# Kernel optimization log

Measured on AMD Instinct MI355X. Metric: run time of the kernel, lower is better.

## Reference

```python
import jax, jax.numpy as jnp
import numpy as np

# ---- module hyperparameters (from init_kwargs) ----
N_REPL = 4      # n
NUM_FM = 32
D = 2
PRD = 2
K_SZ = 2 * D + 1
ALPHA = 0.1
ETA = 0.1
THETA = 0.1
EPS = 1e-10


def symm_pad(x, p):
    # faithful to torch symm_pad: sequential in-place border reflection
    x = x.at[..., :p, :].set(jnp.flip(x[..., p:2 * p, :], axis=-2))
    x = x.at[..., -p:, :].set(jnp.flip(x[..., -2 * p:-p, :], axis=-2))
    x = x.at[..., :, :p].set(jnp.flip(x[..., :, p:2 * p], axis=-1))
    x = x.at[..., :, -p:].set(jnp.flip(x[..., :, -2 * p:-p], axis=-1))
    return x


def pad_activations(A, prd=PRD, d=D):
    H, W = A.shape[-2], A.shape[-1]
    pz = jnp.zeros(A.shape[:-2] + (prd * d + H, prd * d + W), A.dtype)
    pz = pz.at[..., prd:-prd, prd:-prd].set(A)
    return symm_pad(pz, 2 * prd)


def minmax_on_fm(x):
    # min-max normalize each feature map (last two dims) to [0,1]
    mn = x.min(axis=(-2, -1), keepdims=True)
    mx = x.max(axis=(-2, -1), keepdims=True)
    return (x - mn) / (mx - mn + EPS)


def softmax_on_fm(x):
    sh = x.shape
    return jax.nn.softmax(x.reshape(sh[:-2] + (-1,)), axis=-1).reshape(sh)


def softmax_minmax_scaled(x):
    return softmax_on_fm(minmax_on_fm(x))


def conv2d(x, w):
    # x: (B, Cin, H, W), w: (Cout, Cin, k, k), valid conv
    return jax.lax.conv_general_dilated(
        x, w, window_strides=(1, 1), padding='VALID',
        dimension_numbers=('NCHW', 'OIHW', 'NCHW'))


def setup_inputs() -> dict:
    key = jax.random.key(0)
    kA, kK, kN = jax.random.split(key, 3)
    C = N_REPL * NUM_FM
    A = jax.random.uniform(kA, (16, NUM_FM, 56, 56), jnp.float32)
    # K initialized as softmax_on_fm(rand), matching __init__
    K = softmax_on_fm(jax.random.uniform(kK, (C, C, K_SZ, K_SZ), jnp.float32))
    noise = jax.random.normal(kN, (16, C, 56, 56), jnp.float32)
    return {"A": A, "K": K, "noise": noise}


def reference(A, K, noise):
    B, num_fm, H, W = A.shape
    n, d, prd, k = N_REPL, D, PRD, K_SZ
    C = n * num_fm

    A = symm_pad(A, prd)                              # (B, num_fm, H, W)
    Ab = jnp.tile(A, (1, n, 1, 1))                    # (B, C, H, W)
    Ab = jnp.clip(Ab + ETA * noise, 0.0)
    pA = pad_activations(Ab)                          # (B, C, H+4, W+4)

    # torch does K.transpose_(0,1) in place; K1 is the post-transpose K
    K1 = jnp.swapaxes(K, 0, 1)
    L = conv2d(pA, minmax_on_fm(K1)) / num_fm         # (B, C, H, W)
    L = softmax_minmax_scaled(L)

    # winner-take-all across the n replicas of each feature map
    s = (Ab + L).sum(axis=(-2, -1)).reshape(B, n, num_fm)
    winners = jnp.argmax(jnp.swapaxes(s, 1, 2), axis=-1)          # (B, num_fm)
    fm_idx = num_fm * winners + jnp.arange(num_fm)                # (B, num_fm)
    win_mask = jnp.zeros((B, C), Ab.dtype).at[
        jnp.arange(B)[:, None], fm_idx].set(1.0)                  # 1 at winning channels

    # ---- Hebbian K update: per-offset masked cross-correlation ----
    Am = Ab * win_mask[:, :, None, None]  # zero losing *source* channels
    cols = []
    for x in range(k):
        xo = -d + x
        rows = []
        for y in range(k):
            yo = -d + y
            src = Am[:, :, max(0, xo):H + min(xo, 0), max(0, yo):W + min(yo, 0)]
            tgt = Ab[:, :, max(0, -xo):H + min(-xo, 0), max(0, -yo):W + min(-yo, 0)]
            rows.append(jnp.einsum('bchw,bahw->ca', src, tgt) / (C * B))
        cols.append(jnp.stack(rows, axis=-1))        # (C, C, k) over y
    K_change = jnp.stack(cols, axis=-2)              # (C, C, k, k) indexed [c,a,x,y]

    K2 = (1.0 - ALPHA) * K1 + ALPHA * minmax_on_fm(K_change)

    # ---- second lateral pass with losing channels zeroed ----
    A2 = Ab * win_mask[:, :, None, None]
    # torch zeroes only diagonal filters K[c,c] of losing c per sample; since the
    # corresponding input channels of A2 are exactly zero, a single shared-weight
    # conv is mathematically identical.
    L2 = conv2d(pad_activations(A2), minmax_on_fm(jnp.swapaxes(K2, 0, 1))) / num_fm

    gather = lambda X: jnp.take_along_axis(X, fm_idx[:, :, None, None], axis=1)
    O = gather(A2) + THETA * gather(L2)              # (B, num_fm, H, W)
    return O
```

## Files before the change

### kernel.cpp

```cpp
#include <hip/hip_runtime.h>


typedef __attribute__((ext_vector_type(8))) short short8;
typedef __attribute__((ext_vector_type(4))) float floatx4;

#define EPSF 1e-10f

__device__ __forceinline__ int map60(int r) {
  return r < 4 ? 5 - r : (r < 56 ? r - 2 : 109 - r);
}
__device__ __forceinline__ unsigned short f2bf(float x) {
  unsigned int u = __float_as_uint(x);
  u += 0x7fff + ((u >> 16) & 1);
  return (unsigned short)(u >> 16);
}
__device__ __forceinline__ float bf2f(unsigned int h) {
  return __uint_as_float((h & 0xffffu) << 16);
}
__device__ __forceinline__ short8 u4_to_s8(uint4 v) {
  union { uint4 u; short8 s; } cv;
  cv.u = v;
  return cv.s;
}

__global__ __launch_bounds__(256) void k1_build(const float* __restrict__ A,
                                                const float* __restrict__ noise,
                                                unsigned short* __restrict__ Abf,
                                                float* __restrict__ s) {
  int bc = blockIdx.x;
  int b = bc >> 7, c = bc & 127;
  int fm = c & 31;
  const float* Abase = A + (size_t)(b * 32 + fm) * 3136;
  const float* nz = noise + (size_t)bc * 3136;
  unsigned short* outb = Abf + 256 + (size_t)bc * 3840;
  float local = 0.f;
  for (int q = threadIdx.x; q < 960; q += 256) {
    int r = q >> 4, qc = q & 15, col0 = qc << 2;
    int h = r - 2;
    float v0, v1, v2, v3;
    if (r < 2 || r > 57 || qc == 15) {
      v0 = v1 = v2 = v3 = 0.f;
    } else if (r >= 4 && r <= 55 && qc >= 1 && qc <= 13) {
      int w0 = col0 - 2;
      const float* ap = Abase + h * 56 + w0;
      const float* np = nz + h * 56 + w0;
      float2 a0 = *reinterpret_cast<const float2*>(ap);
      float2 a1 = *reinterpret_cast<const float2*>(ap + 2);
      float2 n0 = *reinterpret_cast<const float2*>(np);
      float2 n1 = *reinterpret_cast<const float2*>(np + 2);
      v0 = fmaxf(a0.x + 0.1f * n0.x, 0.f);
      v1 = fmaxf(a0.y + 0.1f * n0.y, 0.f);
      v2 = fmaxf(a1.x + 0.1f * n1.x, 0.f);
      v3 = fmaxf(a1.y + 0.1f * n1.y, 0.f);
    } else {
      float vv[4];
      int hh = h < 2 ? 3 - h : (h >= 54 ? 107 - h : h);
#pragma unroll
      for (int j = 0; j < 4; j++) {
        int w = col0 + j - 2;
        float v = 0.f;
        if ((unsigned)w < 56u) {
          int ww = w < 2 ? 3 - w : (w >= 54 ? 107 - w : w);
          v = fmaxf(Abase[hh * 56 + ww] + 0.1f * nz[h * 56 + w], 0.f);
        }
        vv[j] = v;
      }
      v0 = vv[0]; v1 = vv[1]; v2 = vv[2]; v3 = vv[3];
    }
    local += v0 + v1 + v2 + v3;
    uint2 w;
    w.x = (unsigned)f2bf(v0) | ((unsigned)f2bf(v1) << 16);
    w.y = (unsigned)f2bf(v2) | ((unsigned)f2bf(v3) << 16);
    *reinterpret_cast<uint2*>(outb + r * 64 + col0) = w;
  }
  int lane = threadIdx.x & 63, wid = threadIdx.x >> 6;
  float v = local;
  for (int off = 32; off; off >>= 1) v += __shfl_down(v, off, 64);
  __shared__ float red[4];
  if (lane == 0) red[wid] = v;
  __syncthreads();
  if (threadIdx.x == 0) s[bc] = red[0] + red[1] + red[2] + red[3];
}

__global__ __launch_bounds__(512) void k2_winners(const float* __restrict__ s,
                                                  int* __restrict__ fm_idx,
                                                  int* __restrict__ cmask,
                                                  unsigned short* __restrict__ Abf) {
  int t = threadIdx.x;
  {
    int b = t >> 5, f = t & 31;
    float best = s[b * 128 + f];
    int bn = 0;
    for (int n = 1; n < 4; n++) {
      float v = s[b * 128 + n * 32 + f];
      if (v > best) { best = v; bn = n; }
    }
    fm_idx[t] = bn * 32 + f;
  }
  if (t < 256) Abf[t] = 0;
  if (t >= 256) Abf[256 + 7864320 + (t - 256)] = 0;
  __syncthreads();
  if (t < 128) {
    int m = 0;
    for (int b = 0; b < 16; b++)
      if (fm_idx[b * 32 + (t & 31)] == t) m |= (1 << b);
    cmask[t] = m;
  }
}

__global__ __launch_bounds__(256) void k2t_transpose(const unsigned short* __restrict__ Abf,
                                                     const int* __restrict__ fm_idx,
                                                     unsigned short* __restrict__ T) {
  __shared__ int win[32];
  int b = blockIdx.x / 15, chunk = blockIdx.x % 15;
  if (threadIdx.x < 32) win[threadIdx.x] = fm_idx[b * 32 + threadIdx.x];
  __syncthreads();
  int p = chunk * 256 + threadIdx.x;
  int r = p >> 6, s2 = p & 63;
  int mr = map60(r) + 2;
  int ms = (s2 < 60) ? map60(s2) + 2 : -1;
  unsigned int out[16];
#pragma unroll
  for (int gp = 0; gp < 16; gp++) {
    unsigned short v0 = 0, v1 = 0;
    if (ms >= 0) {
      v0 = Abf[256 + ((size_t)(b * 128) + win[2 * gp]) * 3840 + mr * 64 + ms];
      v1 = Abf[256 + ((size_t)(b * 128) + win[2 * gp + 1]) * 3840 + mr * 64 + ms];
    }
    out[gp] = (unsigned)v0 | ((unsigned)v1 << 16);
  }
  uint4* dst = reinterpret_cast<uint4*>(T + (size_t)b * 122880 + (size_t)p * 32);
#pragma unroll
  for (int q = 0; q < 4; q++) {
    uint4 u;
    u.x = out[4 * q]; u.y = out[4 * q + 1]; u.z = out[4 * q + 2]; u.w = out[4 * q + 3];
    dst[q] = u;
  }
}

__global__ __launch_bounds__(256) void k3_mfma(const unsigned short* __restrict__ Abf,
                                               const int* __restrict__ fm_idx,
                                               float* __restrict__ Kc_b) {
  int bx = blockIdx.x;
  int b = bx & 15;
  int rr = bx >> 4;
  int kh = rr & 1, mt = (rr >> 1) & 1, nt = rr >> 2;
  int wave = threadIdx.x >> 6, lane = threadIdx.x & 63;
  int al = lane & 15, quad = lane >> 4;
  int g0 = mt * 16, a0 = nt * 16;
  int k0 = kh * 1920 + wave * 480;
  floatx4 acc[5][5];
#pragma unroll
  for (int i = 0; i < 5; i++)
#pragma unroll
    for (int j = 0; j < 5; j++) acc[i][j] = (floatx4){0.f, 0.f, 0.f, 0.f};
  int c = fm_idx[b * 32 + g0 + al];
  const unsigned short* pA = Abf + 256 + (size_t)(b * 128 + c) * 3840 + k0 + quad * 8;
  const unsigned short* pB = Abf + 256 + (size_t)(b * 128 + a0 + al) * 3840 + k0 + quad * 8;
  for (int ks = 0; ks < 15; ks++) {
    short8 afr = *reinterpret_cast<const short8*>(pA);
#pragma unroll
    for (int dj = 0; dj < 5; dj++) {
      const unsigned short* bb = pB + 64 * (dj - 2);
      uint2 L = *reinterpret_cast<const uint2*>(bb - 4);
      uint4 M = *reinterpret_cast<const uint4*>(bb);
      uint2 R = *reinterpret_cast<const uint2*>(bb + 8);
      unsigned ab0 = __builtin_amdgcn_alignbit(M.x, L.y, 16);
      unsigned ab1 = __builtin_amdgcn_alignbit(M.y, M.x, 16);
      unsigned ab2 = __builtin_amdgcn_alignbit(M.z, M.y, 16);
      unsigned ab3 = __builtin_amdgcn_alignbit(M.w, M.z, 16);
      unsigned ab4 = __builtin_amdgcn_alignbit(R.x, M.w, 16);
      acc[0][dj] = __builtin_amdgcn_mfma_f32_16x16x32_bf16(
          afr, u4_to_s8((uint4){L.y, M.x, M.y, M.z}), acc[0][dj], 0, 0, 0);
      acc[1][dj] = __builtin_amdgcn_mfma_f32_16x16x32_bf16(
          afr, u4_to_s8((uint4){ab0, ab1, ab2, ab3}), acc[1][dj], 0, 0, 0);
      acc[2][dj] = __builtin_amdgcn_mfma_f32_16x16x32_bf16(
          afr, u4_to_s8((uint4){M.x, M.y, M.z, M.w}), acc[2][dj], 0, 0, 0);
      acc[3][dj] = __builtin_amdgcn_mfma_f32_16x16x32_bf16(
          afr, u4_to_s8((uint4){ab1, ab2, ab3, ab4}), acc[3][dj], 0, 0, 0);
      acc[4][dj] = __builtin_amdgcn_mfma_f32_16x16x32_bf16(
          afr, u4_to_s8((uint4){M.y, M.z, M.w, R.x}), acc[4][dj], 0, 0, 0);
    }
    pA += 32;
    pB += 32;
  }
  __shared__ float red[6400];
  float* myrow = red + lane * 100;
  if (wave == 0) {
#pragma unroll
    for (int di = 0; di < 5; di++)
#pragma unroll
      for (int dj = 0; dj < 5; dj++)
#pragma unroll
        for (int r = 0; r < 4; r++) myrow[(di * 5 + dj) * 4 + r] = acc[di][dj][r];
  }
  __syncthreads();
#pragma unroll
  for (int w = 1; w < 4; w++) {
    if (wave == w) {
#pragma unroll
      for (int di = 0; di < 5; di++)
#pragma unroll
        for (int dj = 0; dj < 5; dj++)
#pragma unroll
          for (int r = 0; r < 4; r++) myrow[(di * 5 + dj) * 4 + r] += acc[di][dj][r];
    }
    __syncthreads();
  }
  if (wave == 0) {
    int slot = b * 2 + kh;
#pragma unroll
    for (int di = 0; di < 5; di++)
#pragma unroll
      for (int dj = 0; dj < 5; dj++) {
        int t_out = 24 - (dj * 5 + di);
#pragma unroll
        for (int r = 0; r < 4; r++) {
          int g = g0 + quad * 4 + r;
          Kc_b[(((size_t)slot * 32 + g) * 128 + (a0 + al)) * 25 + t_out] =
              myrow[(di * 5 + dj) * 4 + r] * (1.0f / 2048.0f);
        }
      }
  }
}

__global__ __launch_bounds__(256) void k4_weights(const float* __restrict__ Kc_b,
                                                  const float* __restrict__ K,
                                                  const int* __restrict__ cmask,
                                                  unsigned short* __restrict__ W2g) {
  int gid = blockIdx.x * 256 + threadIdx.x;
  int o = gid >> 7, i = gid & 127;
  int mi = cmask[i], mo = cmask[o];
  float kc[25];
#pragma unroll
  for (int t = 0; t < 25; t++) kc[t] = 0.f;
  for (int slot = 0; slot < 32; slot++) {
    if ((mi >> (slot >> 1)) & 1) {
      const float* p = Kc_b + (((size_t)slot * 32 + (i & 31)) * 128 + o) * 25;
#pragma unroll
      for (int t = 0; t < 25; t++) kc[t] += p[t];
    }
  }
  float mn = 1e30f, mx = -1e30f;
#pragma unroll
  for (int t = 0; t < 25; t++) { mn = fminf(mn, kc[t]); mx = fmaxf(mx, kc[t]); }
  float d1 = mx - mn + EPSF;
  const float* kp = K + ((size_t)o * 128 + i) * 25;
  float k2[25], mn2 = 1e30f, mx2 = -1e30f;
#pragma unroll
  for (int t = 0; t < 25; t++) {
    k2[t] = 0.9f * kp[t] + 0.1f * ((kc[t] - mn) / d1);
    mn2 = fminf(mn2, k2[t]);
    mx2 = fmaxf(mx2, k2[t]);
  }
  float d2 = mx2 - mn2 + EPSF;
  unsigned short wb[25];
#pragma unroll
  for (int t = 0; t < 25; t++) wb[t] = f2bf((k2[t] - mn2) / d2);
  int mw = mo & mi;
  int f = o & 31, g = i & 31;
  while (mw) {
    int b = __ffs(mw) - 1;
    mw &= mw - 1;
    unsigned short* dst = W2g + ((size_t)(b * 25) * 32 + f) * 32 + g;
#pragma unroll
    for (int t = 0; t < 25; t++) dst[(size_t)t * 1024] = wb[t];
  }
}

__global__ __launch_bounds__(64) void k5_mfma(const unsigned short* __restrict__ W2g,
                                              const unsigned short* __restrict__ T,
                                              const unsigned short* __restrict__ Abf,
                                              const int* __restrict__ fm_idx,
                                              float* __restrict__ O) {
  int bx = blockIdx.x;
  int rg = bx % 14;
  int mtb = bx / 14;
  int mt = mtb & 1, b = mtb >> 1;
  int lane = threadIdx.x, al = lane & 15, quad = lane >> 4;
  int fm = mt * 16 + al;
  short8 afr[25];
#pragma unroll
  for (int t = 0; t < 25; t++)
    afr[t] = *reinterpret_cast<const short8*>(
        W2g + ((size_t)((b * 25 + t) * 32 + fm) << 5) + quad * 8);
  int orow[4];
#pragma unroll
  for (int r = 0; r < 4; r++) orow[r] = fm_idx[b * 32 + mt * 16 + quad * 4 + r];
  const unsigned short* Tb = T + (size_t)b * 122880;
  for (int rr = 0; rr < 4; rr++) {
    int row = 2 + rg * 4 + rr;
    for (int pair = 0; pair < 2; pair++) {
      int px0 = row * 64 + pair * 32 + al;
      floatx4 acca = (floatx4){0.f, 0.f, 0.f, 0.f};
      floatx4 accb = (floatx4){0.f, 0.f, 0.f, 0.f};
#pragma unroll
      for (int t = 0; t < 25; t++) {
        int off = (t / 5 - 2) * 64 + (t % 5) - 2;
        const short8* pb = reinterpret_cast<const short8*>(
            Tb + (ptrdiff_t)(px0 + off) * 32 + quad * 8);
        short8 b0 = pb[0];
        short8 b1 = pb[64];
        acca = __builtin_amdgcn_mfma_f32_16x16x32_bf16(afr[t], b0, acca, 0, 0, 0);
        accb = __builtin_amdgcn_mfma_f32_16x16x32_bf16(afr[t], b1, accb, 0, 0, 0);
      }
      int h = row - 2;
#pragma unroll
      for (int half = 0; half < 2; half++) {
        floatx4 acc = half ? accb : acca;
        int cc = pair * 32 + half * 16 + al;
        if (cc >= 2 && cc < 58) {
          int w = cc - 2;
          int px = row * 64 + cc;
#pragma unroll
          for (int r = 0; r < 4; r++) {
            int f = mt * 16 + quad * 4 + r;
            float base = bf2f(Abf[256 + (size_t)(b * 128 + orow[r]) * 3840 + px]);
            O[(size_t)(b * 32 + f) * 3136 + h * 56 + w] = base + acc[r] * (0.1f / 32.0f);
          }
        }
      }
    }
  }
}

extern "C" void kernel_launch(void* const* d_in, const int* in_sizes, int n_in,
                              void* d_out, int out_size, void* d_ws, size_t ws_size,
                              hipStream_t stream) {
  const float* A = (const float*)d_in[0];
  const float* K = (const float*)d_in[1];
  const float* noise = (const float*)d_in[2];
  float* O = (float*)d_out;

  float* ws = (float*)d_ws;
  unsigned short* Abf = (unsigned short*)ws;
  float* s = ws + 3932416;
  int* fm_idx = (int*)(ws + 3934464);
  int* cmask = (int*)(ws + 3934976);
  float* Kc_b = ws + 3935104;
  unsigned short* T = (unsigned short*)(ws + 7211904);
  unsigned short* W2g = (unsigned short*)(ws + 8194944);

  k1_build<<<2048, 256, 0, stream>>>(A, noise, Abf, s);
  k2_winners<<<1, 512, 0, stream>>>(s, fm_idx, cmask, Abf);
  k2t_transpose<<<240, 256, 0, stream>>>(Abf, fm_idx, T);
  k3_mfma<<<512, 256, 0, stream>>>(Abf, fm_idx, Kc_b);
  k4_weights<<<64, 256, 0, stream>>>(Kc_b, K, cmask, W2g);
  k5_mfma<<<448, 64, 0, stream>>>(W2g, T, Abf, fm_idx, O);
}
```

Baseline: 186.5 us.

## Reuse B-window registers across k-steps in correlation MFMA kernel

Exploits the fact that the 5 row-shifted B windows overlap across consecutive k-steps (stride 32 vs row stride 64): keeps even/odd register windows, shifts them down every two steps and loads only one new row pair, instead of reloading all five windows every step. Also prefetches the next A fragment, fully unrolls the k-loop and sets launch_bounds min 2 blocks. Cuts global/L1 load traffic in exchange for much higher register pressure (60 window regs plus 100 accumulators), which may cause spills or lower occupancy.

New measurement: 196.7 us. 5.5% more time.

```diff
diff --git a/kernel.cpp b/kernel.cpp
--- a/kernel.cpp
+++ b/kernel.cpp
@@ -138,13 +138,13 @@
   }
 }
 
-__global__ __launch_bounds__(256) void k3_mfma(const unsigned short* __restrict__ Abf,
-                                               const int* __restrict__ fm_idx,
-                                               float* __restrict__ Kc_b) {
+__global__ __launch_bounds__(256, 2) void k3_mfma(const unsigned short* __restrict__ Abf,
+                                                  const int* __restrict__ fm_idx,
+                                                  float* __restrict__ Kc_b) {
   int bx = blockIdx.x;
   int b = bx & 15;
-  int rr = bx >> 4;
-  int kh = rr & 1, mt = (rr >> 1) & 1, nt = rr >> 2;
+  int rblk = bx >> 4;
+  int kh = rblk & 1, mt = (rblk >> 1) & 1, nt = rblk >> 2;
   int wave = threadIdx.x >> 6, lane = threadIdx.x & 63;
   int al = lane & 15, quad = lane >> 4;
   int g0 = mt * 16, a0 = nt * 16;
@@ -155,35 +155,65 @@
 #pragma unroll
     for (int j = 0; j < 5; j++) acc[i][j] = (floatx4){0.f, 0.f, 0.f, 0.f};
   int c = fm_idx[b * 32 + g0 + al];
-  const unsigned short* pA = Abf + 256 + (size_t)(b * 128 + c) * 3840 + k0 + quad * 8;
-  const unsigned short* pB = Abf + 256 + (size_t)(b * 128 + a0 + al) * 3840 + k0 + quad * 8;
-  for (int ks = 0; ks < 15; ks++) {
-    short8 afr = *reinterpret_cast<const short8*>(pA);
+  const unsigned short* pA0 = Abf + 256 + (size_t)(b * 128 + c) * 3840 + k0 + quad * 8;
+  const unsigned short* pB0 = Abf + 256 + (size_t)(b * 128 + a0 + al) * 3840 + k0 + quad * 8;
+
+  auto loadwin = [&](unsigned* W, const unsigned short* ptr) {
+    W[0] = *reinterpret_cast<const unsigned*>(ptr - 2);
+    uint4 m = *reinterpret_cast<const uint4*>(ptr);
+    W[1] = m.x; W[2] = m.y; W[3] = m.z; W[4] = m.w;
+    W[5] = *reinterpret_cast<const unsigned*>(ptr + 8);
+  };
+  auto dostep = [&](unsigned (&W)[5][6], short8 afr) {
 #pragma unroll
     for (int dj = 0; dj < 5; dj++) {
-      const unsigned short* bb = pB + 64 * (dj - 2);
-      uint2 L = *reinterpret_cast<const uint2*>(bb - 4);
-      uint4 M = *reinterpret_cast<const uint4*>(bb);
-      uint2 R = *reinterpret_cast<const uint2*>(bb + 8);
-      unsigned ab0 = __builtin_amdgcn_alignbit(M.x, L.y, 16);
-      unsigned ab1 = __builtin_amdgcn_alignbit(M.y, M.x, 16);
-      unsigned ab2 = __builtin_amdgcn_alignbit(M.z, M.y, 16);
-      unsigned ab3 = __builtin_amdgcn_alignbit(M.w, M.z, 16);
-      unsigned ab4 = __builtin_amdgcn_alignbit(R.x, M.w, 16);
+      unsigned d0 = W[dj][0], d1 = W[dj][1], d2 = W[dj][2], d3 = W[dj][3],
+               d4 = W[dj][4], d5 = W[dj][5];
+      unsigned ab0 = __builtin_amdgcn_alignbit(d1, d0, 16);
+      unsigned ab1 = __builtin_amdgcn_alignbit(d2, d1, 16);
+      unsigned ab2 = __builtin_amdgcn_alignbit(d3, d2, 16);
+      unsigned ab3 = __builtin_amdgcn_alignbit(d4, d3, 16);
+      unsigned ab4 = __builtin_amdgcn_alignbit(d5, d4, 16);
       acc[0][dj] = __builtin_amdgcn_mfma_f32_16x16x32_bf16(
-          afr, u4_to_s8((uint4){L.y, M.x, M.y, M.z}), acc[0][dj], 0, 0, 0);
+          afr, u4_to_s8((uint4){d0, d1, d2, d3}), acc[0][dj], 0, 0, 0);
       acc[1][dj] = __builtin_amdgcn_mfma_f32_16x16x32_bf16(
           afr, u4_to_s8((uint4){ab0, ab1, ab2, ab3}), acc[1][dj], 0, 0, 0);
       acc[2][dj] = __builtin_amdgcn_mfma_f32_16x16x32_bf16(
-          afr, u4_to_s8((uint4){M.x, M.y, M.z, M.w}), acc[2][dj], 0, 0, 0);
+          afr, u4_to_s8((uint4){d1, d2, d3, d4}), acc[2][dj], 0, 0, 0);
       acc[3][dj] = __builtin_amdgcn_mfma_f32_16x16x32_bf16(
           afr, u4_to_s8((uint4){ab1, ab2, ab3, ab4}), acc[3][dj], 0, 0, 0);
       acc[4][dj] = __builtin_amdgcn_mfma_f32_16x16x32_bf16(
-          afr, u4_to_s8((uint4){M.y, M.z, M.w, R.x}), acc[4][dj], 0, 0, 0);
-    }
-    pA += 32;
-    pB += 32;
-  }
+          afr, u4_to_s8((uint4){d2, d3, d4, d5}), acc[4][dj], 0, 0, 0);
+    }
+  };
+
+  unsigned We[5][6], Wo[5][6];
+#pragma unroll
+  for (int j = 0; j < 5; j++) {
+    loadwin(We[j], pB0 + 64 * (j - 2));
+    loadwin(Wo[j], pB0 + 64 * (j - 2) + 32);
+  }
+  short8 afr = *reinterpret_cast<const short8*>(pA0);
+#pragma unroll
+  for (int ks = 0; ks < 15; ks++) {
+    short8 afr_n = afr;
+    if (ks < 14) afr_n = *reinterpret_cast<const short8*>(pA0 + 32 * (ks + 1));
+    if (ks & 1) dostep(Wo, afr); else dostep(We, afr);
+    if (ks & 1) {
+      int t = ks >> 1;
+#pragma unroll
+      for (int j = 0; j < 4; j++)
+#pragma unroll
+        for (int d = 0; d < 6; d++) {
+          We[j][d] = We[j + 1][d];
+          Wo[j][d] = Wo[j + 1][d];
+        }
+      loadwin(We[4], pB0 + 64 * (t + 3));
+      loadwin(Wo[4], pB0 + 64 * (t + 3) + 32);
+    }
+    afr = afr_n;
+  }
+
   __shared__ float red[6400];
   float* myrow = red + lane * 100;
   if (wave == 0) {
```

## Software-pipeline k3_mfma loads and move shift windows to the A operand

Applied to the files above, without the earlier changes.

Restructures the k3_mfma inner loop to prefetch the next k-step's operands into registers while issuing the current step's MFMAs, and fully unrolls the 15-step loop. The horizontal shift windows are now built once per step from a single wider A load, with five unshifted B loads, instead of three unaligned B loads plus alignbit shuffles for each dj. It also adds a launch-bounds hint of 2 blocks per SIMD-group. The aim is to hide global load latency and cut redundant loads and ALU work, at the cost of more live registers, which may cause spills or limit occupancy.

Result: faster. 161.1 us (-13.6%).

```diff
diff --git a/kernel.cpp b/kernel.cpp
--- a/kernel.cpp
+++ b/kernel.cpp
@@ -138,13 +138,13 @@
   }
 }
 
-__global__ __launch_bounds__(256) void k3_mfma(const unsigned short* __restrict__ Abf,
-                                               const int* __restrict__ fm_idx,
-                                               float* __restrict__ Kc_b) {
+__global__ __launch_bounds__(256, 2) void k3_mfma(const unsigned short* __restrict__ Abf,
+                                                  const int* __restrict__ fm_idx,
+                                                  float* __restrict__ Kc_b) {
   int bx = blockIdx.x;
   int b = bx & 15;
-  int rr = bx >> 4;
-  int kh = rr & 1, mt = (rr >> 1) & 1, nt = rr >> 2;
+  int rblk = bx >> 4;
+  int kh = rblk & 1, mt = (rblk >> 1) & 1, nt = rblk >> 2;
   int wave = threadIdx.x >> 6, lane = threadIdx.x & 63;
   int al = lane & 15, quad = lane >> 4;
   int g0 = mt * 16, a0 = nt * 16;
@@ -157,33 +157,53 @@
   int c = fm_idx[b * 32 + g0 + al];
   const unsigned short* pA = Abf + 256 + (size_t)(b * 128 + c) * 3840 + k0 + quad * 8;
   const unsigned short* pB = Abf + 256 + (size_t)(b * 128 + a0 + al) * 3840 + k0 + quad * 8;
+
+  auto loadA = [](unsigned* W, const unsigned short* ptr) {
+    W[0] = *reinterpret_cast<const unsigned*>(ptr - 2);
+    uint4 m = *reinterpret_cast<const uint4*>(ptr);
+    W[1] = m.x; W[2] = m.y; W[3] = m.z; W[4] = m.w;
+    W[5] = *reinterpret_cast<const unsigned*>(ptr + 8);
+  };
+
+  unsigned Wc[6], Wn[6];
+  short8 Bc[5], Bn[5];
+  loadA(Wc, pA);
+#pragma unroll
+  for (int dj = 0; dj < 5; dj++)
+    Bc[dj] = *reinterpret_cast<const short8*>(pB + 64 * (dj - 2));
+#pragma unroll
   for (int ks = 0; ks < 15; ks++) {
-    short8 afr = *reinterpret_cast<const short8*>(pA);
-#pragma unroll
-    for (int dj = 0; dj < 5; dj++) {
-      const unsigned short* bb = pB + 64 * (dj - 2);
-      uint2 L = *reinterpret_cast<const uint2*>(bb - 4);
-      uint4 M = *reinterpret_cast<const uint4*>(bb);
-      uint2 R = *reinterpret_cast<const uint2*>(bb + 8);
-      unsigned ab0 = __builtin_amdgcn_alignbit(M.x, L.y, 16);
-      unsigned ab1 = __builtin_amdgcn_alignbit(M.y, M.x, 16);
-      unsigned ab2 = __builtin_amdgcn_alignbit(M.z, M.y, 16);
-      unsigned ab3 = __builtin_amdgcn_alignbit(M.w, M.z, 16);
-      unsigned ab4 = __builtin_amdgcn_alignbit(R.x, M.w, 16);
-      acc[0][dj] = __builtin_amdgcn_mfma_f32_16x16x32_bf16(
-          afr, u4_to_s8((uint4){L.y, M.x, M.y, M.z}), acc[0][dj], 0, 0, 0);
-      acc[1][dj] = __builtin_amdgcn_mfma_f32_16x16x32_bf16(
-          afr, u4_to_s8((uint4){ab0, ab1, ab2, ab3}), acc[1][dj], 0, 0, 0);
-      acc[2][dj] = __builtin_amdgcn_mfma_f32_16x16x32_bf16(
-          afr, u4_to_s8((uint4){M.x, M.y, M.z, M.w}), acc[2][dj], 0, 0, 0);
-      acc[3][dj] = __builtin_amdgcn_mfma_f32_16x16x32_bf16(
-          afr, u4_to_s8((uint4){ab1, ab2, ab3, ab4}), acc[3][dj], 0, 0, 0);
-      acc[4][dj] = __builtin_amdgcn_mfma_f32_16x16x32_bf16(
-          afr, u4_to_s8((uint4){M.y, M.z, M.w, R.x}), acc[4][dj], 0, 0, 0);
-    }
-    pA += 32;
-    pB += 32;
-  }
+    if (ks < 14) {
+      loadA(Wn, pA + 32 * (ks + 1));
+#pragma unroll
+      for (int dj = 0; dj < 5; dj++)
+        Bn[dj] = *reinterpret_cast<const short8*>(pB + 64 * (dj - 2) + 32 * (ks + 1));
+    }
+    unsigned a10 = __builtin_amdgcn_alignbit(Wc[1], Wc[0], 16);
+    unsigned a21 = __builtin_amdgcn_alignbit(Wc[2], Wc[1], 16);
+    unsigned a32 = __builtin_amdgcn_alignbit(Wc[3], Wc[2], 16);
+    unsigned a43 = __builtin_amdgcn_alignbit(Wc[4], Wc[3], 16);
+    unsigned a54 = __builtin_amdgcn_alignbit(Wc[5], Wc[4], 16);
+    short8 afr[5];
+    afr[0] = u4_to_s8((uint4){Wc[2], Wc[3], Wc[4], Wc[5]});
+    afr[1] = u4_to_s8((uint4){a21, a32, a43, a54});
+    afr[2] = u4_to_s8((uint4){Wc[1], Wc[2], Wc[3], Wc[4]});
+    afr[3] = u4_to_s8((uint4){a10, a21, a32, a43});
+    afr[4] = u4_to_s8((uint4){Wc[0], Wc[1], Wc[2], Wc[3]});
+#pragma unroll
+    for (int di = 0; di < 5; di++)
+#pragma unroll
+      for (int dj = 0; dj < 5; dj++)
+        acc[di][dj] =
+            __builtin_amdgcn_mfma_f32_16x16x32_bf16(afr[di], Bc[dj], acc[di][dj], 0, 0, 0);
+    if (ks < 14) {
+#pragma unroll
+      for (int d = 0; d < 6; d++) Wc[d] = Wn[d];
+#pragma unroll
+      for (int dj = 0; dj < 5; dj++) Bc[dj] = Bn[dj];
+    }
+  }
+
   __shared__ float red[6400];
   float* myrow = red + lane * 100;
   if (wave == 0) {
```
